# Kernel tuning notes

Hardware: AMD Instinct MI355X
Metric: run time of the kernel (lower is better)

The kernel has to match this reference:

```python
import jax, jax.numpy as jnp
import numpy as np

N_LAYERS = 4
D_MODEL = 256
P = 128            # ssm_size // 2 (conj_sym S5)
LATENT_DIM = 256
MAX_SEQ_LEN = 32768
OUTPUT_DIM = 64
LN_EPS = 1e-6      # flax nn.LayerNorm default


def layer_norm(x, scale, bias):
    mu = jnp.mean(x, axis=-1, keepdims=True)
    var = jnp.mean(jnp.square(x - mu), axis=-1, keepdims=True)
    return (x - mu) * jax.lax.rsqrt(var + LN_EPS) * scale + bias


def s5_ssm(u, Lre, Lim, Bre, Bim, Cre, Cim, Dvec, log_step, resets):
    """u: (L, H) float. Returns (L, H) float. conj_sym S5, zoh discretization."""
    step = jnp.exp(log_step)                       # (P,)
    Lam = Lre + 1j * Lim                           # (P,) complex
    Lam_bar = jnp.exp(Lam * step)                  # (P,)
    B_bar = ((Lam_bar - 1.0) / Lam)[:, None] * (Bre + 1j * Bim)  # (P, H)
    Bu = u @ B_bar.T                               # (L, P) complex
    A = jnp.broadcast_to(Lam_bar, Bu.shape)        # (L, P)
    c = resets[:, None].astype(u.dtype)            # (L, 1)

    def binop(qi, qj):
        Ai, bi, ci = qi
        Aj, bj, cj = qj
        return (Aj * Ai * (1.0 - cj) + Aj * cj,
                (Aj * bi + bj) * (1.0 - cj) + bj * cj,
                ci * (1.0 - cj) + cj)

    # zero initial hidden state => no prepend needed (identical result)
    _, xs, _ = jax.lax.associative_scan(binop, (A, Bu, c))
    y = 2.0 * jnp.real(xs @ (Cre + 1j * Cim).T)    # (L, H), conj_sym doubling
    return y + u * Dvec


def setup_inputs() -> dict:
    key = jax.random.key(0)
    ks = jax.random.split(key, 16)
    f = jax.random.normal
    return {
        "latent": f(ks[0], (LATENT_DIM,), jnp.float32),
        "W_expand": f(ks[1], (LATENT_DIM, D_MODEL), jnp.float32) / np.sqrt(LATENT_DIM),
        "b_expand": jnp.zeros((D_MODEL,), jnp.float32),
        "norm_scale": jnp.ones((N_LAYERS, D_MODEL), jnp.float32),
        "norm_bias": jnp.zeros((N_LAYERS, D_MODEL), jnp.float32),
        "Lambda_re": -(0.1 + 0.9 * jax.random.uniform(ks[2], (N_LAYERS, P))),
        "Lambda_im": np.pi * f(ks[3], (N_LAYERS, P), jnp.float32),
        "B_re": f(ks[4], (N_LAYERS, P, D_MODEL), jnp.float32) / np.sqrt(D_MODEL),
        "B_im": f(ks[5], (N_LAYERS, P, D_MODEL), jnp.float32) / np.sqrt(D_MODEL),
        "C_re": f(ks[6], (N_LAYERS, D_MODEL, P), jnp.float32) / np.sqrt(P),
        "C_im": f(ks[7], (N_LAYERS, D_MODEL, P), jnp.float32) / np.sqrt(P),
        "D": f(ks[8], (N_LAYERS, D_MODEL), jnp.float32),
        "log_step": jnp.log(jax.random.uniform(ks[9], (N_LAYERS, P), minval=1e-3, maxval=1e-1)),
        "W1": f(ks[10], (N_LAYERS, D_MODEL, D_MODEL), jnp.float32) / np.sqrt(D_MODEL),
        "b1": jnp.zeros((N_LAYERS, D_MODEL), jnp.float32),
        "W2": f(ks[11], (N_LAYERS, D_MODEL, D_MODEL), jnp.float32) / np.sqrt(D_MODEL),
        "b2": jnp.zeros((N_LAYERS, D_MODEL), jnp.float32),
        "W_out": f(ks[12], (D_MODEL, OUTPUT_DIM), jnp.float32) / np.sqrt(D_MODEL),
        "b_out": jnp.zeros((OUTPUT_DIM,), jnp.float32),
        "seq_len": MAX_SEQ_LEN,
    }


def reference(latent, W_expand, b_expand, norm_scale, norm_bias,
              Lambda_re, Lambda_im, B_re, B_im, C_re, C_im, D, log_step,
              W1, b1, W2, b2, W_out, b_out, seq_len):
    # latent_expand + leaky_relu, then broadcast to full trajectory
    x = jax.nn.leaky_relu(latent @ W_expand + b_expand)        # (H,)
    x = jnp.broadcast_to(x[None, :], (MAX_SEQ_LEN, D_MODEL))    # (L, H); batch dim of 1 dropped
    resets = jnp.zeros((MAX_SEQ_LEN,), x.dtype)                 # dones = zeros
    for i in range(N_LAYERS):
        skip = x
        h = layer_norm(x, norm_scale[i], norm_bias[i])          # prenorm
        y = s5_ssm(h, Lambda_re[i], Lambda_im[i], B_re[i], B_im[i],
                   C_re[i], C_im[i], D[i], log_step[i], resets)
        y = layer_norm(y, norm_scale[i], norm_bias[i])          # gtrxl norm (shared params)
        y = jax.nn.gelu(y)
        y = (y @ W1[i] + b1[i]) * jax.nn.sigmoid(y @ W2[i] + b2[i])  # full_glu
        x = skip + y
    return x @ W_out + b_out                                    # (L, output_dim)
```

## Files before the change

kernel.cpp:

```cpp
#include <hip/hip_runtime.h>
#include <stdint.h>

#define LSEQ 32768
#define NCH 512
#define TCH 64

typedef _Float16 half8 __attribute__((ext_vector_type(8)));
typedef _Float16 half4v __attribute__((ext_vector_type(4)));
typedef _Float16 half2v __attribute__((ext_vector_type(2)));
typedef float f32x4 __attribute__((ext_vector_type(4)));
typedef float f32x2 __attribute__((ext_vector_type(2)));

__device__ __forceinline__ float sigmoidf_(float x) { return 1.f / (1.f + __expf(-x)); }
__device__ __forceinline__ float gelu_(float x) {
    float z = 0.7978845608028654f * (x + 0.044715f * x * x * x);
    float e = __expf(2.f * z);
    float t = 1.f - 2.f / (e + 1.f);
    return 0.5f * x * (1.f + t);
}

__device__ __forceinline__ void gll16(const _Float16* gp, _Float16* lp) {
    __builtin_amdgcn_global_load_lds((__attribute__((address_space(1))) void*)gp,
                                     (__attribute__((address_space(3))) void*)lp, 16, 0, 0);
}

template <int BM, int BN, int BK, int WR, int WC>
__device__ __forceinline__ void gemm_core(const _Float16* __restrict__ A,
                                          const _Float16* __restrict__ Wt,
                                          _Float16* sA, _Float16* sW,
                                          int m0, int n0,
                                          f32x4 (&acc)[BM / (WR * 16)][BN / (WC * 16)]) {
    constexpr int MT = BM / (WR * 16);
    constexpr int NT = BN / (WC * 16);
    constexpr int KS = BK / 32;
    constexpr int CA = KS * (BM / 16);
    constexpr int CW = KS * (BN / 16);
    constexpr int NKB = 256 / BK;
    constexpr int NWAVE = WR * WC;
    const int tid = threadIdx.x;
    const int wid = tid >> 6;
    const int lane = tid & 63;
    const int wm = wid / WC;
    const int wn = wid % WC;

    f32x4 zero = {0.f, 0.f, 0.f, 0.f};
#pragma unroll
    for (int i = 0; i < MT; ++i)
#pragma unroll
        for (int j = 0; j < NT; ++j) acc[i][j] = zero;

    auto stage = [&](int kb, int buf) {
#pragma unroll
        for (int i = 0; i < CA / NWAVE; ++i) {
            int c = i * NWAVE + wid;
            int ks = c / (BM / 16), r16 = c % (BM / 16);
            const _Float16* gp = A + (m0 + r16 * 16 + (lane & 15)) * 256 + kb + ks * 32 + (lane >> 4) * 8;
            gll16(gp, sA + buf * (CA * 512) + c * 512);
        }
#pragma unroll
        for (int i = 0; i < CW / NWAVE; ++i) {
            int c = i * NWAVE + wid;
            int ks = c / (BN / 16), n16 = c % (BN / 16);
            const _Float16* gp = Wt + (n0 + n16 * 16 + (lane & 15)) * 256 + kb + ks * 32 + (lane >> 4) * 8;
            gll16(gp, sW + buf * (CW * 512) + c * 512);
        }
    };

    stage(0, 0);
#pragma unroll
    for (int t = 0; t < NKB; ++t) {
        __syncthreads();
        if (t + 1 < NKB) stage((t + 1) * BK, (t + 1) & 1);
        const _Float16* bA = sA + (t & 1) * (CA * 512);
        const _Float16* bW = sW + (t & 1) * (CW * 512);
#pragma unroll
        for (int ks = 0; ks < KS; ++ks) {
            half8 af[MT], bf[NT];
#pragma unroll
            for (int mt = 0; mt < MT; ++mt)
                af[mt] = *(const half8*)(bA + (ks * (BM / 16) + wm * MT + mt) * 512 + lane * 8);
#pragma unroll
            for (int nt = 0; nt < NT; ++nt)
                bf[nt] = *(const half8*)(bW + (ks * (BN / 16) + wn * NT + nt) * 512 + lane * 8);
#pragma unroll
            for (int mt = 0; mt < MT; ++mt)
#pragma unroll
                for (int nt = 0; nt < NT; ++nt)
                    acc[mt][nt] = __builtin_amdgcn_mfma_f32_16x16x32_f16(af[mt], bf[nt], acc[mt][nt], 0, 0, 0);
        }
    }
    __syncthreads();
}

__global__ __launch_bounds__(512) void s5_k0a(const float* __restrict__ lre, const float* __restrict__ lim,
                                              const float* __restrict__ lstep,
                                              float* aR, float* aI, float* cbR, float* cbI,
                                              float* aTR, float* aTI, float* alp, float* ralp) {
    int i = threadIdx.x;
    float st = expf(lstep[i]);
    float lr = lre[i] * st, li = lim[i] * st;
    float ea = expf(lr);
    float ar = ea * cosf(li), ai = ea * sinf(li);
    float den = lre[i] * lre[i] + lim[i] * lim[i];
    float nr = ar - 1.f, ni = ai;
    float cr = (nr * lre[i] + ni * lim[i]) / den;
    float ci = (ni * lre[i] - nr * lim[i]) / den;
    float cm = sqrtf(cr * cr + ci * ci);
    float al = sqrtf(2.83f / fmaxf(cm, 1e-8f));
    float eT = expf(lr * (float)TCH);
    aR[i] = ar; aI[i] = ai;
    cbR[i] = cr; cbI[i] = ci;
    aTR[i] = eT * cosf(li * (float)TCH);
    aTI[i] = eT * sinf(li * (float)TCH);
    alp[i] = al; ralp[i] = 1.f / al;
}

__global__ __launch_bounds__(256) void s5_k0b(const float* __restrict__ Bre, const float* __restrict__ Bim,
                                              const float* __restrict__ Cre, const float* __restrict__ Cim,
                                              const float* __restrict__ W1, const float* __restrict__ W2,
                                              const float* __restrict__ b1, const float* __restrict__ b2,
                                              const float* __restrict__ Wout,
                                              const float* __restrict__ cbR, const float* __restrict__ cbI,
                                              const float* __restrict__ alp, const float* __restrict__ ralp,
                                              _Float16* Wbu, _Float16* Wc, _Float16* Wglu,
                                              _Float16* WoutT, float* bglu) {
    int stride = gridDim.x * blockDim.x;
    int tid0 = blockIdx.x * blockDim.x + threadIdx.x;
    for (int i = tid0; i < 262144; i += stride) {
        int l = i >> 16, n = (i >> 8) & 255, k = i & 255;
        int s = n >> 4, lmn = n & 15;
        int p = l * 128 + (s >> 1) * 16 + lmn;
        float re = cbR[p] * Bre[p * 256 + k] - cbI[p] * Bim[p * 256 + k];
        float im = cbR[p] * Bim[p * 256 + k] + cbI[p] * Bre[p * 256 + k];
        Wbu[i] = (_Float16)(((s & 1) ? im : re) * alp[p]);
    }
    for (int i = tid0; i < 262144; i += stride) {
        int l = i >> 16, n = (i >> 8) & 255, k = i & 255;
        int p = k >> 1;
        float base = (k & 1) ? -2.f * Cim[(l * 256 + n) * 128 + p]
                             : 2.f * Cre[(l * 256 + n) * 128 + p];
        Wc[i] = (_Float16)(base * ralp[l * 128 + p]);
    }
    for (int i = tid0; i < 524288; i += stride) {
        int l = i >> 17, n = (i >> 8) & 511, k = i & 255;
        int j = ((n >> 7) << 6) | (((n >> 6) & 1) << 5) | (((n >> 5) & 1) << 4) | (n & 15);
        const float* src = ((n >> 4) & 1) ? W2 : W1;
        Wglu[i] = (_Float16)src[(l * 256 + k) * 256 + j];
    }
    for (int i = tid0; i < 16384; i += stride) {
        int n = i >> 8, k = i & 255;
        WoutT[i] = (_Float16)Wout[k * 64 + n];
    }
    for (int i = tid0; i < 2048; i += stride) {
        int l = i >> 9, n = i & 511;
        int j = ((n >> 7) << 6) | (((n >> 6) & 1) << 5) | (((n >> 5) & 1) << 4) | (n & 15);
        bglu[i] = (((n >> 4) & 1) ? b2 : b1)[l * 256 + j];
    }
}

__global__ __launch_bounds__(256) void s5_k0c(const float* __restrict__ latent, const float* __restrict__ W,
                                              const float* __restrict__ b, float* __restrict__ x0) {
    __shared__ float lat[256];
    lat[threadIdx.x] = latent[threadIdx.x];
    __syncthreads();
    float s = b[threadIdx.x];
    for (int k = 0; k < 256; ++k) s += lat[k] * W[k * 256 + threadIdx.x];
    x0[threadIdx.x] = (s > 0.f) ? s : 0.01f * s;
}

__global__ __launch_bounds__(256) void s5_k1_fill(const float* __restrict__ x0, float* __restrict__ x) {
    int i = blockIdx.x * 256 + threadIdx.x;
    f32x4 v = *(const f32x4*)(x0 + (i & 63) * 4);
    *(f32x4*)(x + i * 4) = v;
}

__global__ __launch_bounds__(512, 2) void s5_k3_lngemm(const float* __restrict__ x,
                                                       const _Float16* __restrict__ Wt,
                                                       const float* __restrict__ gamma,
                                                       const float* __restrict__ beta,
                                                       _Float16* __restrict__ h,
                                                       _Float16* __restrict__ Buh) {
    __shared__ _Float16 sW[64 * 512];
    int tid = threadIdx.x, wid = tid >> 6, lane = tid & 63;
    int lm = lane & 15, quad = lane >> 4;
    int m0 = blockIdx.x * 128;
    int rowb = m0 + wid * 16;

    auto stageW = [&](int half) {
#pragma unroll
        for (int i = 0; i < 8; ++i) {
            int c = i * 8 + wid;
            int ks = c >> 3, n16 = c & 7;
            gll16(Wt + (half * 128 + n16 * 16 + lm) * 256 + ks * 32 + quad * 8, sW + c * 512);
        }
    };
    stageW(0);

    int row = rowb + lm;
    half8 af[8];
    {
        f32x4 v[16];
#pragma unroll
        for (int ks = 0; ks < 8; ++ks) {
            v[2 * ks]     = *(const f32x4*)(x + row * 256 + ks * 32 + quad * 8);
            v[2 * ks + 1] = *(const f32x4*)(x + row * 256 + ks * 32 + quad * 8 + 4);
        }
        float s1 = 0.f, s2 = 0.f;
#pragma unroll
        for (int i = 0; i < 16; ++i)
#pragma unroll
            for (int j = 0; j < 4; ++j) { float t = v[i][j]; s1 += t; s2 += t * t; }
        s1 += __shfl_xor(s1, 16, 64); s2 += __shfl_xor(s2, 16, 64);
        s1 += __shfl_xor(s1, 32, 64); s2 += __shfl_xor(s2, 32, 64);
        float mu = s1 * (1.f / 256.f);
        float var = s2 * (1.f / 256.f) - mu * mu;
        float rs = rsqrtf(fmaxf(var, 0.f) + 1e-6f);
#pragma unroll
        for (int ks = 0; ks < 8; ++ks) {
            f32x4 g0 = *(const f32x4*)(gamma + ks * 32 + quad * 8);
            f32x4 g1 = *(const f32x4*)(gamma + ks * 32 + quad * 8 + 4);
            f32x4 b0 = *(const f32x4*)(beta + ks * 32 + quad * 8);
            f32x4 b1 = *(const f32x4*)(beta + ks * 32 + quad * 8 + 4);
            half8 o;
#pragma unroll
            for (int j = 0; j < 4; ++j) {
                o[j]     = (_Float16)((v[2 * ks][j] - mu) * rs * g0[j] + b0[j]);
                o[j + 4] = (_Float16)((v[2 * ks + 1][j] - mu) * rs * g1[j] + b1[j]);
            }
            af[ks] = o;
            *(half8*)(h + row * 256 + ks * 32 + quad * 8) = o;
        }
    }
    asm volatile("s_waitcnt vmcnt(0)" ::: "memory");
    __syncthreads();

    f32x4 zero = {0.f, 0.f, 0.f, 0.f};
    f32x4 acc[2][8];
#pragma unroll
    for (int hf = 0; hf < 2; ++hf)
#pragma unroll
        for (int nt = 0; nt < 8; ++nt) acc[hf][nt] = zero;

#pragma unroll
    for (int ks = 0; ks < 8; ++ks) {
        half8 bf[8];
#pragma unroll
        for (int nt = 0; nt < 8; ++nt)
            bf[nt] = *(const half8*)(sW + (ks * 8 + nt) * 512 + lane * 8);
#pragma unroll
        for (int nt = 0; nt < 8; ++nt)
            acc[0][nt] = __builtin_amdgcn_mfma_f32_16x16x32_f16(af[ks], bf[nt], acc[0][nt], 0, 0, 0);
    }
    __syncthreads();
    stageW(1);
    asm volatile("s_waitcnt vmcnt(0)" ::: "memory");
    __syncthreads();
#pragma unroll
    for (int ks = 0; ks < 8; ++ks) {
        half8 bf[8];
#pragma unroll
        for (int nt = 0; nt < 8; ++nt)
            bf[nt] = *(const half8*)(sW + (ks * 8 + nt) * 512 + lane * 8);
#pragma unroll
        for (int nt = 0; nt < 8; ++nt)
            acc[1][nt] = __builtin_amdgcn_mfma_f32_16x16x32_f16(af[ks], bf[nt], acc[1][nt], 0, 0, 0);
    }

#pragma unroll
    for (int u = 0; u < 8; ++u) {
        int hf = u >> 2, q = u & 3;
        int p = u * 16 + lm;
#pragma unroll
        for (int r = 0; r < 4; ++r) {
            half2v o = {(_Float16)acc[hf][2 * q][r], (_Float16)acc[hf][2 * q + 1][r]};
            *(half2v*)(Buh + (rowb + quad * 4 + r) * 256 + 2 * p) = o;
        }
    }
}

__global__ __launch_bounds__(128, 4) void s5_k4_scan(const _Float16* __restrict__ Bu,
                                                     const float* __restrict__ aR, const float* __restrict__ aI,
                                                     _Float16* __restrict__ xsh,
                                                     float* __restrict__ carRI) {
    int p = threadIdx.x, c = blockIdx.x;
    float ar = aR[p], ai = aI[p];
    int t0 = c * TCH;
    const _Float16* bp = Bu + t0 * 256 + 2 * p;
    _Float16* xp = xsh + t0 * 256 + 2 * p;
    half2v b0[16], b1[16];
    float sr = 0.f, si = 0.f;

    auto loadg = [&](half2v (&buf)[16], int g) {
#pragma unroll
        for (int j = 0; j < 16; ++j) buf[j] = *(const half2v*)(bp + (g * 16 + j) * 256);
    };
    auto procg = [&](half2v (&buf)[16], int g) {
#pragma unroll
        for (int j = 0; j < 16; ++j) {
            float nr = fmaf(ar, sr, fmaf(-ai, si, (float)buf[j][0]));
            float ni = fmaf(ar, si, fmaf(ai, sr, (float)buf[j][1]));
            sr = nr; si = ni;
            *(half2v*)(xp + (g * 16 + j) * 256) = half2v{(_Float16)sr, (_Float16)si};
        }
    };
    loadg(b0, 0);
    loadg(b1, 1);
    procg(b0, 0);
    loadg(b0, 2);
    procg(b1, 1);
    loadg(b1, 3);
    procg(b0, 2);
    procg(b1, 3);
    *(f32x2*)(carRI + (c * 128 + p) * 2) = f32x2{sr, si};
}

__global__ __launch_bounds__(128, 4) void s5_k6_apply(const _Float16* __restrict__ xsh,
                                                      const float* __restrict__ carRI,
                                                      const float* __restrict__ aR, const float* __restrict__ aI,
                                                      const float* __restrict__ aTR, const float* __restrict__ aTI,
                                                      _Float16* __restrict__ xs2) {
    int p = threadIdx.x, c = blockIdx.x;
    int t0 = c * TCH;
    const _Float16* xp = xsh + t0 * 256 + 2 * p;
    half2v hv[TCH];
#pragma unroll
    for (int j = 0; j < TCH; ++j) hv[j] = *(const half2v*)(xp + j * 256);
    float tr = aTR[p], ti = aTI[p];
    float cr = 0.f, ci = 0.f;
#pragma unroll 8
    for (int i = 0; i < c; ++i) {
        f32x2 w = *(const f32x2*)(carRI + (i * 128 + p) * 2);
        float nr = fmaf(tr, cr, fmaf(-ti, ci, w[0]));
        float ni = fmaf(tr, ci, fmaf(ti, cr, w[1]));
        cr = nr; ci = ni;
    }
    float ar = aR[p], ai = aI[p];
    float fr = ar, fi = ai;
    _Float16* op = xs2 + t0 * 256 + 2 * p;
#pragma unroll
    for (int j = 0; j < TCH; ++j) {
        float xr = (float)hv[j][0] + fr * cr - fi * ci;
        float xi = (float)hv[j][1] + fr * ci + fi * cr;
        *(half2v*)(op + j * 256) = half2v{(_Float16)xr, (_Float16)xi};
        float nr = fr * ar - fi * ai, ni = fr * ai + fi * ar;
        fr = nr; fi = ni;
    }
}

__global__ __launch_bounds__(512, 2) void s5_k7_gemm_c(const _Float16* __restrict__ A,
                                                       const _Float16* __restrict__ Wt,
                                                       const _Float16* __restrict__ h,
                                                       const float* __restrict__ Dv,
                                                       const float* __restrict__ gamma,
                                                       const float* __restrict__ beta,
                                                       _Float16* __restrict__ g) {
    __shared__ _Float16 sW[64 * 512];
    int tid = threadIdx.x, wid = tid >> 6, lane = tid & 63;
    int lm = lane & 15, quad = lane >> 4;
    int m0 = blockIdx.x * 128;
    int rowb = m0 + wid * 16;

    auto stageW = [&](int half) {
#pragma unroll
        for (int i = 0; i < 8; ++i) {
            int c = i * 8 + wid;
            int ks = c >> 3, n16 = c & 7;
            gll16(Wt + (half * 128 + n16 * 16 + lm) * 256 + ks * 32 + quad * 8, sW + c * 512);
        }
    };
    stageW(0);
    half8 af[8];
#pragma unroll
    for (int ks = 0; ks < 8; ++ks)
        af[ks] = *(const half8*)(A + (rowb + lm) * 256 + ks * 32 + quad * 8);
    asm volatile("s_waitcnt vmcnt(0)" ::: "memory");
    __syncthreads();

    f32x4 zero = {0.f, 0.f, 0.f, 0.f};
    f32x4 acc[2][8];
#pragma unroll
    for (int hf = 0; hf < 2; ++hf)
#pragma unroll
        for (int nt = 0; nt < 8; ++nt) acc[hf][nt] = zero;

#pragma unroll
    for (int ks = 0; ks < 8; ++ks) {
        half8 bf[8];
#pragma unroll
        for (int nt = 0; nt < 8; ++nt)
            bf[nt] = *(const half8*)(sW + (ks * 8 + nt) * 512 + lane * 8);
#pragma unroll
        for (int nt = 0; nt < 8; ++nt)
            acc[0][nt] = __builtin_amdgcn_mfma_f32_16x16x32_f16(af[ks], bf[nt], acc[0][nt], 0, 0, 0);
    }
    __syncthreads();
    stageW(1);
    asm volatile("s_waitcnt vmcnt(0)" ::: "memory");
    __syncthreads();
#pragma unroll
    for (int ks = 0; ks < 8; ++ks) {
        half8 bf[8];
#pragma unroll
        for (int nt = 0; nt < 8; ++nt)
            bf[nt] = *(const half8*)(sW + (ks * 8 + nt) * 512 + lane * 8);
#pragma unroll
        for (int nt = 0; nt < 8; ++nt)
            acc[1][nt] = __builtin_amdgcn_mfma_f32_16x16x32_f16(af[ks], bf[nt], acc[1][nt], 0, 0, 0);
    }

#pragma unroll
    for (int hf = 0; hf < 2; ++hf)
#pragma unroll
        for (int nt = 0; nt < 8; ++nt) {
            int col = hf * 128 + nt * 16 + lm;
            float dv = Dv[col];
#pragma unroll
            for (int r = 0; r < 4; ++r)
                acc[hf][nt][r] += (float)h[(rowb + quad * 4 + r) * 256 + col] * dv;
        }
    float mu[4], rs[4];
#pragma unroll
    for (int r = 0; r < 4; ++r) {
        float a = 0.f, b = 0.f;
#pragma unroll
        for (int hf = 0; hf < 2; ++hf)
#pragma unroll
            for (int nt = 0; nt < 8; ++nt) {
                float v = acc[hf][nt][r];
                a += v; b += v * v;
            }
#pragma unroll
        for (int off = 1; off < 16; off <<= 1) {
            a += __shfl_xor(a, off, 64);
            b += __shfl_xor(b, off, 64);
        }
        float m = a * (1.f / 256.f);
        float var = b * (1.f / 256.f) - m * m;
        mu[r] = m;
        rs[r] = rsqrtf(fmaxf(var, 0.f) + 1e-6f);
    }
#pragma unroll
    for (int hf = 0; hf < 2; ++hf)
#pragma unroll
        for (int nt = 0; nt < 8; ++nt) {
            int col = hf * 128 + nt * 16 + lm;
            float ga = gamma[col], be = beta[col];
#pragma unroll
            for (int r = 0; r < 4; ++r) {
                float hn = (acc[hf][nt][r] - mu[r]) * rs[r] * ga + be;
                g[(rowb + quad * 4 + r) * 256 + col] = (_Float16)gelu_(hn);
            }
        }
}

__global__ __launch_bounds__(256, 2) void s5_k8_gemm_glu(const _Float16* __restrict__ A,
                                                         const _Float16* __restrict__ Wt,
                                                         const float* __restrict__ bias,
                                                         float* __restrict__ x,
                                                         _Float16* __restrict__ xh,
                                                         int wxh) {
    __shared__ _Float16 sW[64 * 512];
    int tid = threadIdx.x, wid = tid >> 6, lane = tid & 63;
    int lm = lane & 15, quad = lane >> 4;
    int n0 = blockIdx.y * 128;
    int m0 = blockIdx.x * 128;
#pragma unroll
    for (int i = 0; i < 16; ++i) {
        int c = i * 4 + wid;
        int ks = c >> 3, n16 = c & 7;
        gll16(Wt + (n0 + n16 * 16 + lm) * 256 + ks * 32 + quad * 8, sW + c * 512);
    }
    int rowb = m0 + wid * 32;
    half8 af[2][8];
#pragma unroll
    for (int mt = 0; mt < 2; ++mt)
#pragma unroll
        for (int ks = 0; ks < 8; ++ks)
            af[mt][ks] = *(const half8*)(A + (rowb + mt * 16 + lm) * 256 + ks * 32 + quad * 8);
    asm volatile("s_waitcnt vmcnt(0)" ::: "memory");
    __syncthreads();

    f32x4 zero = {0.f, 0.f, 0.f, 0.f};
    f32x4 acc[2][8];
#pragma unroll
    for (int mt = 0; mt < 2; ++mt)
#pragma unroll
        for (int nt = 0; nt < 8; ++nt) acc[mt][nt] = zero;
#pragma unroll
    for (int ks = 0; ks < 8; ++ks) {
        half8 bf[8];
#pragma unroll
        for (int nt = 0; nt < 8; ++nt)
            bf[nt] = *(const half8*)(sW + (ks * 8 + nt) * 512 + lane * 8);
#pragma unroll
        for (int mt = 0; mt < 2; ++mt)
#pragma unroll
            for (int nt = 0; nt < 8; ++nt)
                acc[mt][nt] = __builtin_amdgcn_mfma_f32_16x16x32_f16(af[mt][ks], bf[nt], acc[mt][nt], 0, 0, 0);
    }
    int jbase = (n0 >> 1) + lm;
    float xold[2][4][4];
#pragma unroll
    for (int mt = 0; mt < 2; ++mt)
#pragma unroll
        for (int q = 0; q < 4; ++q)
#pragma unroll
            for (int r = 0; r < 4; ++r)
                xold[mt][q][r] = x[(rowb + mt * 16 + quad * 4 + r) * 256 + jbase + q * 16];
#pragma unroll
    for (int mt = 0; mt < 2; ++mt)
#pragma unroll
        for (int q = 0; q < 4; ++q) {
            float b1v = bias[n0 + (2 * q) * 16 + lm];
            float b2v = bias[n0 + (2 * q + 1) * 16 + lm];
            int jcol = jbase + q * 16;
#pragma unroll
            for (int r = 0; r < 4; ++r) {
                float u1 = acc[mt][2 * q][r] + b1v;
                float u2 = acc[mt][2 * q + 1][r] + b2v;
                float gl = u1 * sigmoidf_(u2);
                int idx = (rowb + mt * 16 + quad * 4 + r) * 256 + jcol;
                float xn = xold[mt][q][r] + gl;
                x[idx] = xn;
                if (wxh) xh[idx] = (_Float16)xn;
            }
        }
}

__global__ __launch_bounds__(256) void s5_k9_gemm_out(const _Float16* __restrict__ A,
                                                      const _Float16* __restrict__ Wt,
                                                      const float* __restrict__ bout,
                                                      float* __restrict__ out) {
    __shared__ _Float16 sA[2 * 16 * 512], sW[2 * 8 * 512];
    f32x4 acc[2][4];
    int m0 = blockIdx.x * 128;
    gemm_core<128, 64, 64, 4, 1>(A, Wt, sA, sW, m0, 0, acc);
    int tid = threadIdx.x, wid = tid >> 6, lane = tid & 63, lm = lane & 15, quad = lane >> 4;
#pragma unroll
    for (int mt = 0; mt < 2; ++mt)
#pragma unroll
        for (int nt = 0; nt < 4; ++nt) {
            int col = nt * 16 + lm;
            float bv = bout[col];
#pragma unroll
            for (int r = 0; r < 4; ++r) {
                int row = m0 + wid * 32 + mt * 16 + quad * 4 + r;
                out[row * 64 + col] = acc[mt][nt][r] + bv;
            }
        }
}

constexpr size_t OFF_X    = 0;
constexpr size_t OFF_BU   = 33554432;
constexpr size_t OFF_H    = 67108864;
constexpr size_t OFF_XSH  = 83886080;
constexpr size_t OFF_WBU  = 100663296;
constexpr size_t OFF_WC   = OFF_WBU + 524288;
constexpr size_t OFF_WGLU = OFF_WC + 524288;
constexpr size_t OFF_WOUT = OFF_WGLU + 1048576;
constexpr size_t OFF_BGLU = OFF_WOUT + 32768;
constexpr size_t OFF_AR   = OFF_BGLU + 8192;
constexpr size_t OFF_AI   = OFF_AR + 2048;
constexpr size_t OFF_CBR  = OFF_AI + 2048;
constexpr size_t OFF_CBI  = OFF_CBR + 2048;
constexpr size_t OFF_ATR  = OFF_CBI + 2048;
constexpr size_t OFF_ATI  = OFF_ATR + 2048;
constexpr size_t OFF_ALP  = OFF_ATI + 2048;
constexpr size_t OFF_RALP = OFF_ALP + 2048;
constexpr size_t OFF_X0   = OFF_RALP + 2048;
constexpr size_t OFF_CARRI= OFF_X0 + 1024;

extern "C" void kernel_launch(void* const* d_in, const int* in_sizes, int n_in,
                              void* d_out, int out_size, void* d_ws, size_t ws_size,
                              hipStream_t stream) {
    (void)in_sizes; (void)n_in; (void)out_size; (void)ws_size;
    const float* latent    = (const float*)d_in[0];
    const float* W_expand  = (const float*)d_in[1];
    const float* b_expand  = (const float*)d_in[2];
    const float* norm_s    = (const float*)d_in[3];
    const float* norm_b    = (const float*)d_in[4];
    const float* Lre       = (const float*)d_in[5];
    const float* Lim       = (const float*)d_in[6];
    const float* Bre       = (const float*)d_in[7];
    const float* Bim       = (const float*)d_in[8];
    const float* Cre       = (const float*)d_in[9];
    const float* Cim       = (const float*)d_in[10];
    const float* Dv        = (const float*)d_in[11];
    const float* lstep     = (const float*)d_in[12];
    const float* W1        = (const float*)d_in[13];
    const float* b1        = (const float*)d_in[14];
    const float* W2        = (const float*)d_in[15];
    const float* b2        = (const float*)d_in[16];
    const float* Wout      = (const float*)d_in[17];
    const float* bout      = (const float*)d_in[18];

    char* ws = (char*)d_ws;
    float*    x    = (float*)(ws + OFF_X);
    _Float16* Buh  = (_Float16*)(ws + OFF_BU);
    _Float16* xs2  = (_Float16*)(ws + OFF_BU);
    _Float16* gbuf = (_Float16*)(ws + OFF_BU + 16777216);
    _Float16* hbuf = (_Float16*)(ws + OFF_H);
    _Float16* xh   = (_Float16*)(ws + OFF_H);
    _Float16* xsh  = (_Float16*)(ws + OFF_XSH);
    _Float16* Wbu  = (_Float16*)(ws + OFF_WBU);
    _Float16* Wc   = (_Float16*)(ws + OFF_WC);
    _Float16* Wglu = (_Float16*)(ws + OFF_WGLU);
    _Float16* WoutT= (_Float16*)(ws + OFF_WOUT);
    float* bglu = (float*)(ws + OFF_BGLU);
    float* aR  = (float*)(ws + OFF_AR);
    float* aI  = (float*)(ws + OFF_AI);
    float* cbR = (float*)(ws + OFF_CBR);
    float* cbI = (float*)(ws + OFF_CBI);
    float* aTR = (float*)(ws + OFF_ATR);
    float* aTI = (float*)(ws + OFF_ATI);
    float* alp = (float*)(ws + OFF_ALP);
    float* ralp= (float*)(ws + OFF_RALP);
    float* x0  = (float*)(ws + OFF_X0);
    float* carRI=(float*)(ws + OFF_CARRI);

    s5_k0a<<<1, 512, 0, stream>>>(Lre, Lim, lstep, aR, aI, cbR, cbI, aTR, aTI, alp, ralp);
    s5_k0b<<<256, 256, 0, stream>>>(Bre, Bim, Cre, Cim, W1, W2, b1, b2, Wout,
                                    cbR, cbI, alp, ralp, Wbu, Wc, Wglu, WoutT, bglu);
    s5_k0c<<<1, 256, 0, stream>>>(latent, W_expand, b_expand, x0);
    s5_k1_fill<<<8192, 256, 0, stream>>>(x0, x);

    for (int l = 0; l < 4; ++l) {
        s5_k3_lngemm<<<256, 512, 0, stream>>>(x, Wbu + l * 65536,
                                              norm_s + l * 256, norm_b + l * 256,
                                              hbuf, Buh);
        s5_k4_scan<<<NCH, 128, 0, stream>>>(Buh, aR + l * 128, aI + l * 128, xsh, carRI);
        s5_k6_apply<<<NCH, 128, 0, stream>>>(xsh, carRI, aR + l * 128, aI + l * 128,
                                             aTR + l * 128, aTI + l * 128, xs2);
        s5_k7_gemm_c<<<256, 512, 0, stream>>>(xs2, Wc + l * 65536, hbuf, Dv + l * 256,
                                              norm_s + l * 256, norm_b + l * 256, gbuf);
        s5_k8_gemm_glu<<<dim3(256, 4), 256, 0, stream>>>(gbuf, Wglu + l * 131072,
                                                         bglu + l * 512, x, xh, (l == 3) ? 1 : 0);
    }
    s5_k9_gemm_out<<<256, 256, 0, stream>>>(xh, WoutT, bout, (float*)d_out);
}
```

Measured before the change: 546.0 us.

## Store residual stream in fp16 and restructure scan as carry-then-rescan

```diff
diff --git a/kernel.cpp b/kernel.cpp
--- a/kernel.cpp
+++ b/kernel.cpp
@@ -159,22 +159,22 @@
 }
 
 __global__ __launch_bounds__(256) void s5_k0c(const float* __restrict__ latent, const float* __restrict__ W,
-                                              const float* __restrict__ b, float* __restrict__ x0) {
+                                              const float* __restrict__ b, _Float16* __restrict__ x0h) {
     __shared__ float lat[256];
     lat[threadIdx.x] = latent[threadIdx.x];
     __syncthreads();
     float s = b[threadIdx.x];
     for (int k = 0; k < 256; ++k) s += lat[k] * W[k * 256 + threadIdx.x];
-    x0[threadIdx.x] = (s > 0.f) ? s : 0.01f * s;
-}
-
-__global__ __launch_bounds__(256) void s5_k1_fill(const float* __restrict__ x0, float* __restrict__ x) {
+    x0h[threadIdx.x] = (_Float16)((s > 0.f) ? s : 0.01f * s);
+}
+
+__global__ __launch_bounds__(256) void s5_k1_fill(const _Float16* __restrict__ x0h, _Float16* __restrict__ x) {
     int i = blockIdx.x * 256 + threadIdx.x;
-    f32x4 v = *(const f32x4*)(x0 + (i & 63) * 4);
-    *(f32x4*)(x + i * 4) = v;
-}
-
-__global__ __launch_bounds__(512, 2) void s5_k3_lngemm(const float* __restrict__ x,
+    half8 v = *(const half8*)(x0h + (i & 31) * 8);
+    *(half8*)(x + i * 8) = v;
+}
+
+__global__ __launch_bounds__(512, 2) void s5_k3_lngemm(const _Float16* __restrict__ x,
                                                        const _Float16* __restrict__ Wt,
                                                        const float* __restrict__ gamma,
                                                        const float* __restrict__ beta,
@@ -199,17 +199,15 @@
     int row = rowb + lm;
     half8 af[8];
     {
-        f32x4 v[16];
-#pragma unroll
-        for (int ks = 0; ks < 8; ++ks) {
-            v[2 * ks]     = *(const f32x4*)(x + row * 256 + ks * 32 + quad * 8);
-            v[2 * ks + 1] = *(const f32x4*)(x + row * 256 + ks * 32 + quad * 8 + 4);
-        }
+        half8 xv[8];
+#pragma unroll
+        for (int ks = 0; ks < 8; ++ks)
+            xv[ks] = *(const half8*)(x + row * 256 + ks * 32 + quad * 8);
         float s1 = 0.f, s2 = 0.f;
 #pragma unroll
-        for (int i = 0; i < 16; ++i)
-#pragma unroll
-            for (int j = 0; j < 4; ++j) { float t = v[i][j]; s1 += t; s2 += t * t; }
+        for (int i = 0; i < 8; ++i)
+#pragma unroll
+            for (int j = 0; j < 8; ++j) { float t = (float)xv[i][j]; s1 += t; s2 += t * t; }
         s1 += __shfl_xor(s1, 16, 64); s2 += __shfl_xor(s2, 16, 64);
         s1 += __shfl_xor(s1, 32, 64); s2 += __shfl_xor(s2, 32, 64);
         float mu = s1 * (1.f / 256.f);
@@ -224,8 +222,8 @@
             half8 o;
 #pragma unroll
             for (int j = 0; j < 4; ++j) {
-                o[j]     = (_Float16)((v[2 * ks][j] - mu) * rs * g0[j] + b0[j]);
-                o[j + 4] = (_Float16)((v[2 * ks + 1][j] - mu) * rs * g1[j] + b1[j]);
+                o[j]     = (_Float16)(((float)xv[ks][j] - mu) * rs * g0[j] + b0[j]);
+                o[j + 4] = (_Float16)(((float)xv[ks][j + 4] - mu) * rs * g1[j] + b1[j]);
             }
             af[ks] = o;
             *(half8*)(h + row * 256 + ks * 32 + quad * 8) = o;
@@ -278,53 +276,37 @@
     }
 }
 
-__global__ __launch_bounds__(128, 4) void s5_k4_scan(const _Float16* __restrict__ Bu,
-                                                     const float* __restrict__ aR, const float* __restrict__ aI,
-                                                     _Float16* __restrict__ xsh,
-                                                     float* __restrict__ carRI) {
+__global__ __launch_bounds__(128, 4) void s5_k4_carry(const _Float16* __restrict__ Bu,
+                                                      const float* __restrict__ aR, const float* __restrict__ aI,
+                                                      float* __restrict__ carRI) {
     int p = threadIdx.x, c = blockIdx.x;
-    float ar = aR[p], ai = aI[p];
     int t0 = c * TCH;
     const _Float16* bp = Bu + t0 * 256 + 2 * p;
-    _Float16* xp = xsh + t0 * 256 + 2 * p;
-    half2v b0[16], b1[16];
+    half2v hv[TCH];
+#pragma unroll
+    for (int j = 0; j < TCH; ++j) hv[j] = *(const half2v*)(bp + j * 256);
+    float ar = aR[p], ai = aI[p];
     float sr = 0.f, si = 0.f;
-
-    auto loadg = [&](half2v (&buf)[16], int g) {
-#pragma unroll
-        for (int j = 0; j < 16; ++j) buf[j] = *(const half2v*)(bp + (g * 16 + j) * 256);
-    };
-    auto procg = [&](half2v (&buf)[16], int g) {
-#pragma unroll
-        for (int j = 0; j < 16; ++j) {
-            float nr = fmaf(ar, sr, fmaf(-ai, si, (float)buf[j][0]));
-            float ni = fmaf(ar, si, fmaf(ai, sr, (float)buf[j][1]));
-            sr = nr; si = ni;
-            *(half2v*)(xp + (g * 16 + j) * 256) = half2v{(_Float16)sr, (_Float16)si};
-        }
-    };
-    loadg(b0, 0);
-    loadg(b1, 1);
-    procg(b0, 0);
-    loadg(b0, 2);
-    procg(b1, 1);
-    loadg(b1, 3);
-    procg(b0, 2);
-    procg(b1, 3);
+#pragma unroll
+    for (int j = 0; j < TCH; ++j) {
+        float nr = fmaf(ar, sr, fmaf(-ai, si, (float)hv[j][0]));
+        float ni = fmaf(ar, si, fmaf(ai, sr, (float)hv[j][1]));
+        sr = nr; si = ni;
+    }
     *(f32x2*)(carRI + (c * 128 + p) * 2) = f32x2{sr, si};
 }
 
-__global__ __launch_bounds__(128, 4) void s5_k6_apply(const _Float16* __restrict__ xsh,
-                                                      const float* __restrict__ carRI,
-                                                      const float* __restrict__ aR, const float* __restrict__ aI,
-                                                      const float* __restrict__ aTR, const float* __restrict__ aTI,
-                                                      _Float16* __restrict__ xs2) {
+__global__ __launch_bounds__(128, 4) void s5_k6_scan(const _Float16* __restrict__ Bu,
+                                                     const float* __restrict__ carRI,
+                                                     const float* __restrict__ aR, const float* __restrict__ aI,
+                                                     const float* __restrict__ aTR, const float* __restrict__ aTI,
+                                                     _Float16* __restrict__ xs2) {
     int p = threadIdx.x, c = blockIdx.x;
     int t0 = c * TCH;
-    const _Float16* xp = xsh + t0 * 256 + 2 * p;
+    const _Float16* bp = Bu + t0 * 256 + 2 * p;
     half2v hv[TCH];
 #pragma unroll
-    for (int j = 0; j < TCH; ++j) hv[j] = *(const half2v*)(xp + j * 256);
+    for (int j = 0; j < TCH; ++j) hv[j] = *(const half2v*)(bp + j * 256);
     float tr = aTR[p], ti = aTI[p];
     float cr = 0.f, ci = 0.f;
 #pragma unroll 8
@@ -335,15 +317,14 @@
         cr = nr; ci = ni;
     }
     float ar = aR[p], ai = aI[p];
-    float fr = ar, fi = ai;
+    float sr = cr, si = ci;
     _Float16* op = xs2 + t0 * 256 + 2 * p;
 #pragma unroll
     for (int j = 0; j < TCH; ++j) {
-        float xr = (float)hv[j][0] + fr * cr - fi * ci;
-        float xi = (float)hv[j][1] + fr * ci + fi * cr;
-        *(half2v*)(op + j * 256) = half2v{(_Float16)xr, (_Float16)xi};
-        float nr = fr * ar - fi * ai, ni = fr * ai + fi * ar;
-        fr = nr; fi = ni;
+        float nr = fmaf(ar, sr, fmaf(-ai, si, (float)hv[j][0]));
+        float ni = fmaf(ar, si, fmaf(ai, sr, (float)hv[j][1]));
+        sr = nr; si = ni;
+        *(half2v*)(op + j * 256) = half2v{(_Float16)sr, (_Float16)si};
     }
 }
 
@@ -456,9 +437,7 @@
 __global__ __launch_bounds__(256, 2) void s5_k8_gemm_glu(const _Float16* __restrict__ A,
                                                          const _Float16* __restrict__ Wt,
                                                          const float* __restrict__ bias,
-                                                         float* __restrict__ x,
-                                                         _Float16* __restrict__ xh,
-                                                         int wxh) {
+                                                         _Float16* __restrict__ x) {
     __shared__ _Float16 sW[64 * 512];
     int tid = threadIdx.x, wid = tid >> 6, lane = tid & 63;
     int lm = lane & 15, quad = lane >> 4;
@@ -499,7 +478,7 @@
                 acc[mt][nt] = __builtin_amdgcn_mfma_f32_16x16x32_f16(af[mt][ks], bf[nt], acc[mt][nt], 0, 0, 0);
     }
     int jbase = (n0 >> 1) + lm;
-    float xold[2][4][4];
+    _Float16 xold[2][4][4];
 #pragma unroll
     for (int mt = 0; mt < 2; ++mt)
 #pragma unroll
@@ -520,9 +499,7 @@
                 float u2 = acc[mt][2 * q + 1][r] + b2v;
                 float gl = u1 * sigmoidf_(u2);
                 int idx = (rowb + mt * 16 + quad * 4 + r) * 256 + jcol;
-                float xn = xold[mt][q][r] + gl;
-                x[idx] = xn;
-                if (wxh) xh[idx] = (_Float16)xn;
+                x[idx] = (_Float16)((float)xold[mt][q][r] + gl);
             }
         }
 }
@@ -553,7 +530,6 @@
 constexpr size_t OFF_X    = 0;
 constexpr size_t OFF_BU   = 33554432;
 constexpr size_t OFF_H    = 67108864;
-constexpr size_t OFF_XSH  = 83886080;
 constexpr size_t OFF_WBU  = 100663296;
 constexpr size_t OFF_WC   = OFF_WBU + 524288;
 constexpr size_t OFF_WGLU = OFF_WC + 524288;
@@ -567,8 +543,8 @@
 constexpr size_t OFF_ATI  = OFF_ATR + 2048;
 constexpr size_t OFF_ALP  = OFF_ATI + 2048;
 constexpr size_t OFF_RALP = OFF_ALP + 2048;
-constexpr size_t OFF_X0   = OFF_RALP + 2048;
-constexpr size_t OFF_CARRI= OFF_X0 + 1024;
+constexpr size_t OFF_X0H  = OFF_RALP + 2048;
+constexpr size_t OFF_CARRI= OFF_X0H + 1024;
 
 extern "C" void kernel_launch(void* const* d_in, const int* in_sizes, int n_in,
                               void* d_out, int out_size, void* d_ws, size_t ws_size,
@@ -595,13 +571,11 @@
     const float* bout      = (const float*)d_in[18];
 
     char* ws = (char*)d_ws;
-    float*    x    = (float*)(ws + OFF_X);
+    _Float16* x    = (_Float16*)(ws + OFF_X);
     _Float16* Buh  = (_Float16*)(ws + OFF_BU);
     _Float16* xs2  = (_Float16*)(ws + OFF_BU);
     _Float16* gbuf = (_Float16*)(ws + OFF_BU + 16777216);
     _Float16* hbuf = (_Float16*)(ws + OFF_H);
-    _Float16* xh   = (_Float16*)(ws + OFF_H);
-    _Float16* xsh  = (_Float16*)(ws + OFF_XSH);
     _Float16* Wbu  = (_Float16*)(ws + OFF_WBU);
     _Float16* Wc   = (_Float16*)(ws + OFF_WC);
     _Float16* Wglu = (_Float16*)(ws + OFF_WGLU);
@@ -615,26 +589,26 @@
     float* aTI = (float*)(ws + OFF_ATI);
     float* alp = (float*)(ws + OFF_ALP);
     float* ralp= (float*)(ws + OFF_RALP);
-    float* x0  = (float*)(ws + OFF_X0);
+    _Float16* x0h = (_Float16*)(ws + OFF_X0H);
     float* carRI=(float*)(ws + OFF_CARRI);
 
     s5_k0a<<<1, 512, 0, stream>>>(Lre, Lim, lstep, aR, aI, cbR, cbI, aTR, aTI, alp, ralp);
     s5_k0b<<<256, 256, 0, stream>>>(Bre, Bim, Cre, Cim, W1, W2, b1, b2, Wout,
                                     cbR, cbI, alp, ralp, Wbu, Wc, Wglu, WoutT, bglu);
-    s5_k0c<<<1, 256, 0, stream>>>(latent, W_expand, b_expand, x0);
-    s5_k1_fill<<<8192, 256, 0, stream>>>(x0, x);
+    s5_k0c<<<1, 256, 0, stream>>>(latent, W_expand, b_expand, x0h);
+    s5_k1_fill<<<4096, 256, 0, stream>>>(x0h, x);
 
     for (int l = 0; l < 4; ++l) {
         s5_k3_lngemm<<<256, 512, 0, stream>>>(x, Wbu + l * 65536,
                                               norm_s + l * 256, norm_b + l * 256,
                                               hbuf, Buh);
-        s5_k4_scan<<<NCH, 128, 0, stream>>>(Buh, aR + l * 128, aI + l * 128, xsh, carRI);
-        s5_k6_apply<<<NCH, 128, 0, stream>>>(xsh, carRI, aR + l * 128, aI + l * 128,
-                                             aTR + l * 128, aTI + l * 128, xs2);
+        s5_k4_carry<<<NCH, 128, 0, stream>>>(Buh, aR + l * 128, aI + l * 128, carRI);
+        s5_k6_scan<<<NCH, 128, 0, stream>>>(Buh, carRI, aR + l * 128, aI + l * 128,
+                                            aTR + l * 128, aTI + l * 128, xs2);
         s5_k7_gemm_c<<<256, 512, 0, stream>>>(xs2, Wc + l * 65536, hbuf, Dv + l * 256,
                                               norm_s + l * 256, norm_b + l * 256, gbuf);
         s5_k8_gemm_glu<<<dim3(256, 4), 256, 0, stream>>>(gbuf, Wglu + l * 131072,
-                                                         bglu + l * 512, x, xh, (l == 3) ? 1 : 0);
-    }
-    s5_k9_gemm_out<<<256, 256, 0, stream>>>(xh, WoutT, bout, (float*)d_out);
-}
+                                                         bglu + l * 512, x);
+    }
+    s5_k9_gemm_out<<<256, 256, 0, stream>>>(x, WoutT, bout, (float*)d_out);
+}
```

Result: faster. 512.1 us, median of 2 (-6.2%).
